# Kernel optimization log

Hardware: AMD Instinct MI355X
Metric: run time of the kernel (lower is better)

The kernel has to match this reference:

```python
import jax, jax.numpy as jnp
import numpy as np

PH, PW = 2, 2
SCALE = (0.5, 0.5)
HARDNESS = 2.0
BN_EPS = 1e-5

def conv2d(x, w, b, pad):
    y = jax.lax.conv_general_dilated(x, w, (1, 1), [(pad, pad), (pad, pad)],
                                     dimension_numbers=('NCHW', 'OIHW', 'NCHW'))
    return y + b[None, :, None, None]

def nearest_resize(x, oh, ow):
    # torch F.interpolate default 'nearest': src_idx = floor(dst_idx * in/out)
    _, _, ih, iw = x.shape
    hi = jnp.floor(jnp.arange(oh) * (ih / oh)).astype(jnp.int32)
    wi = jnp.floor(jnp.arange(ow) * (iw / ow)).astype(jnp.int32)
    return x[:, :, hi][:, :, :, wi]

def bilinear_resize(x, oh, ow):
    # matches torch bilinear align_corners=False (half-pixel, no antialias)
    b, c = x.shape[0], x.shape[1]
    return jax.image.resize(x, (b, c, oh, ow), method='linear', antialias=False)

def grid_sample_bilinear(feat, grid):
    # feat [B,C,H,W], grid [B,gh,gw,2] with (x,y) in [-1,1]; align_corners=False, zeros padding
    B, C, H, W = feat.shape
    gx, gy = grid[..., 0], grid[..., 1]
    ix = (gx + 1.0) * (W * 0.5) - 0.5
    iy = (gy + 1.0) * (H * 0.5) - 0.5
    x0f = jnp.floor(ix); y0f = jnp.floor(iy)
    wx = ix - x0f; wy = iy - y0f
    x0 = x0f.astype(jnp.int32); y0 = y0f.astype(jnp.int32)
    x1 = x0 + 1; y1 = y0 + 1

    def gather(f, yy, xx):
        valid = ((yy >= 0) & (yy < H) & (xx >= 0) & (xx < W)).astype(f.dtype)
        yc = jnp.clip(yy, 0, H - 1); xc = jnp.clip(xx, 0, W - 1)
        return f[:, yc, xc] * valid[None]  # [C,gh,gw]

    def per_sample(f, y0, x0, y1, x1, wx, wy):
        v00 = gather(f, y0, x0); v01 = gather(f, y0, x1)
        v10 = gather(f, y1, x0); v11 = gather(f, y1, x1)
        wx_ = wx[None]; wy_ = wy[None]
        return (v00 * (1 - wx_) * (1 - wy_) + v01 * wx_ * (1 - wy_)
                + v10 * (1 - wx_) * wy_ + v11 * wx_ * wy_)

    return jax.vmap(per_sample)(feat, y0, x0, y1, x1, wx, wy)

def lens_forward(feat, w1, b1, gamma, beta, rmean, rvar, w2, b2):
    B, C, H, W = feat.shape
    dh, dw = H // PH, W // PW
    dsz_h, dsz_w = int(H * SCALE[0]), int(W * SCALE[1])
    # ekern: conv3x3 + BN(eval) + ReLU6
    x = conv2d(feat, w1, b1, 1)
    inv = jax.lax.rsqrt(rvar + BN_EPS)
    x = (x - rmean[None, :, None, None]) * inv[None, :, None, None]
    x = x * gamma[None, :, None, None] + beta[None, :, None, None]
    x = jnp.clip(x, 0.0, 6.0)
    # dkern (eval branch): channel-norm normalize with gating, conv5x5 (no pad) + sigmoid
    nrm = jnp.linalg.norm(x, axis=1, keepdims=True)
    xn = x / (nrm + 9e-8) * (nrm > 0.09).astype(x.dtype)
    dmap_raw = jax.nn.sigmoid(conv2d(xn, w2, b2, 0))  # [B,2,H-4,W-4]
    ndmap = nearest_resize(dmap_raw, dh + 2, dw + 2)
    # dmap += 0.0009; interior += hardness
    mask = jnp.zeros((dh + 2, dw + 2), x.dtype).at[1:-1, 1:-1].set(1.0)
    dmap = ndmap + 0.0009 + HARDNESS * mask[None, None]
    # bilinear round trip through dsz
    dsm = bilinear_resize(dmap, dsz_h, dsz_w)
    dmap = bilinear_resize(dsm, dh + 2, dw + 2)
    # neko_dense_norm: normalize, cumsum -> CDF sampling grid in [-1,1]
    h_ = dmap[:, 0:1]; w_ = dmap[:, 1:2]
    h_ = h_ / jnp.sum(h_, axis=2, keepdims=True)
    w_ = w_ / jnp.sum(w_, axis=3, keepdims=True)
    hc = jnp.cumsum(h_, axis=2); wc = jnp.cumsum(w_, axis=3)
    grid = jnp.concatenate([wc[:, :, 1:-1, 1:-1], hc[:, :, 1:-1, 1:-1]], axis=1) * 2 - 1
    grid = jnp.transpose(grid, (0, 2, 3, 1))  # [B,dh,dw,2] (x,y)
    dst = grid_sample_bilinear(feat, grid)  # [B,C,dh,dw]
    # adaptive_avg_pool2d([dh,dw]) on a [dh,dw] map is identity -> skip
    return dst, dmap

def setup_inputs() -> dict:
    key = jax.random.key(0)
    ks = jax.random.split(key, 9)
    B, ICH, H, W, CH = 16, 64, 256, 256, 64
    feat = jax.random.normal(ks[0], (B, ICH, H, W), jnp.float32)
    w1 = jax.random.normal(ks[1], (CH, ICH, 3, 3), jnp.float32) * 0.05
    b1 = jax.random.normal(ks[2], (CH,), jnp.float32) * 0.05
    gamma = 1.0 + jax.random.normal(ks[3], (CH,), jnp.float32) * 0.05
    beta = jax.random.normal(ks[4], (CH,), jnp.float32) * 0.05
    rmean = jax.random.normal(ks[5], (CH,), jnp.float32) * 0.05
    rvar = jax.random.uniform(ks[6], (CH,), jnp.float32) + 0.5
    w2 = jax.random.normal(ks[7], (2, CH, 5, 5), jnp.float32) * 0.05
    b2 = jax.random.normal(ks[8], (2,), jnp.float32) * 0.05
    return {'feat': feat, 'w1': w1, 'b1': b1, 'gamma': gamma, 'beta': beta,
            'rmean': rmean, 'rvar': rvar, 'w2': w2, 'b2': b2}

def reference(feat, w1, b1, gamma, beta, rmean, rvar, w2, b2):
    dst, dmap = lens_forward(feat, w1, b1, gamma, beta, rmean, rvar, w2, b2)
    return dst, jax.lax.stop_gradient(dmap)
```

## Files before the change

kernel.cpp:

```cpp
#include <hip/hip_runtime.h>
#include <hip/hip_bf16.h>

typedef __hip_bfloat16 bf16;
typedef __attribute__((ext_vector_type(8))) short bf16x8;
typedef __attribute__((ext_vector_type(4))) float f32x4;

static __device__ __forceinline__ ushort f2bf(float f) {
    uint u = __float_as_uint(f);
    u += 0x7fff + ((u >> 16) & 1);
    return (ushort)(u >> 16);
}

static __device__ __forceinline__ void gl_lds16(const void* g, void* l) {
    __builtin_amdgcn_global_load_lds(
        (const __attribute__((address_space(1))) uint*)g,
        (__attribute__((address_space(3))) uint*)l, 16, 0, 0);
}

static __device__ __forceinline__ int xcd_remap(int lid, int nwg) {
    int q = nwg >> 3, r = nwg & 7;
    int xcd = lid & 7, idx = lid >> 3;
    return (xcd < r ? xcd * (q + 1) : r * (q + 1) + (xcd - r) * q) + idx;
}

#define FT_ROW 264
#define FT_IMG ((size_t)258 * 264 * 64)
#define XN_IMG ((size_t)256 * 256 * 64)

__global__ __launch_bounds__(256) void k_wt(const float* __restrict__ w1,
                                            ushort* __restrict__ w_bf) {
    int i = blockIdx.x * 256 + threadIdx.x;
    if (i >= 36864) return;
    int oc = i / 576, rem = i - oc * 576;
    int ic = rem / 9, tap = rem - ic * 9;
    w_bf[tap * 4096 + oc * 64 + (ic ^ ((oc & 7) << 3))] = f2bf(w1[i]);
}

__global__ __launch_bounds__(256) void k_wt2(const float* __restrict__ w2,
                                             ushort* __restrict__ w2_bf) {
    int i = blockIdx.x * 256 + threadIdx.x;
    if (i >= 3200) return;
    int oc = i / 1600, rem = i - oc * 1600;
    int ic = rem / 25, tap = rem - ic * 25;
    w2_bf[(tap * 2 + oc) * 64 + ic] = f2bf(w2[i]);
}

__global__ __launch_bounds__(256) void k_zero(ushort* __restrict__ featT, int nb) {
    int t = blockIdx.x * 256 + threadIdx.x;
    const int per = 1040 * 8;
    if (t >= nb * per) return;
    int b = t / per, u = t - b * per;
    int px = u >> 3, oct = u & 7;
    int yp, xp;
    if (px < 264)       { yp = 0;   xp = px; }
    else if (px < 528)  { yp = 257; xp = px - 264; }
    else { int k = px - 528; yp = 1 + (k >> 1); xp = (k & 1) ? 257 : 0; }
    ushort* p = featT + (size_t)b * FT_IMG + ((size_t)yp * FT_ROW + xp) * 64 + oct * 8;
    *(uint4*)p = make_uint4(0u, 0u, 0u, 0u);
}

__global__ __launch_bounds__(256) void k_tr(const float* __restrict__ feat_c,
                                            ushort* __restrict__ featT) {
    __shared__ ushort s_t[64][72];
    const int b = blockIdx.z, y = blockIdx.y, x0 = blockIdx.x * 64;
    const int t = threadIdx.x;
    const int xl = t & 63, icg = t >> 6;

    const float* fb = feat_c + (size_t)b * 64 * 65536 + (size_t)y * 256 + x0 + xl;
#pragma unroll
    for (int k = 0; k < 16; ++k) {
        int ic = icg * 16 + k;
        s_t[ic][xl] = f2bf(fb[(size_t)ic * 65536]);
    }
    __syncthreads();

    ushort* ob = featT + (size_t)b * FT_IMG + ((size_t)(y + 1) * FT_ROW + (x0 + 1)) * 64;
#pragma unroll
    for (int u2 = 0; u2 < 2; ++u2) {
        int u = u2 * 256 + t;
        int x = u >> 3, oct = u & 7;
        int xp7 = (x + 1) & 7;
        uint p0 = (uint)s_t[oct * 8 + 0][x] | ((uint)s_t[oct * 8 + 1][x] << 16);
        uint p1 = (uint)s_t[oct * 8 + 2][x] | ((uint)s_t[oct * 8 + 3][x] << 16);
        uint p2 = (uint)s_t[oct * 8 + 4][x] | ((uint)s_t[oct * 8 + 5][x] << 16);
        uint p3 = (uint)s_t[oct * 8 + 6][x] | ((uint)s_t[oct * 8 + 7][x] << 16);
        *(uint4*)(ob + (size_t)x * 64 + (oct ^ xp7) * 8) = make_uint4(p0, p1, p2, p3);
    }
}

__global__ __launch_bounds__(256, 2) void k_conv1(
    const ushort* __restrict__ featT, const ushort* __restrict__ w_bf,
    const float* __restrict__ b1, const float* __restrict__ gamma,
    const float* __restrict__ beta, const float* __restrict__ rmean,
    const float* __restrict__ rvar, ushort* __restrict__ xn) {
    __shared__ __align__(16) ushort s_in[6 * 72 * 64];
    __shared__ __align__(16) ushort s_w[12288];
    __shared__ float2 s_bn[64];

    const int lid = blockIdx.x + (blockIdx.y << 2) + (blockIdx.z << 8);
    const int nid = xcd_remap(lid, (int)gridDim.z << 8);
    const int b   = nid >> 8;
    const int x0p = (nid & 3) * 64;
    const int y0  = ((nid >> 2) & 63) * 4;

    const int tid = threadIdx.x;
    const int lane = tid & 63;
    const int w    = tid >> 6;
    const int l15  = lane & 15;
    const int l4   = lane >> 4;

    if (tid < 64) {
        float inv = 1.0f / sqrtf(rvar[tid] + 1e-5f);
        float sA = inv * gamma[tid];
        float sB = (b1[tid] - rmean[tid]) * sA + beta[tid];
        s_bn[tid] = make_float2(sA, sB);
    }

    const ushort* fT = featT + (size_t)b * FT_IMG;
    {
        int aStart = w * 13 + (w < 2 ? w : 2);
        int aCnt   = (w < 2) ? 14 : 13;
        for (int q = 0; q < aCnt; ++q) {
            int o = (aStart + q) * 1024;
            int r = o / 9216;
            int rem = o - r * 9216;
            const ushort* g = fT + ((size_t)(y0 + r) * FT_ROW + x0p) * 64 +
                              (rem >> 1) + lane * 8;
            gl_lds16(g, (char*)s_in + o);
        }
    }

    f32x4 acc[4][4];
#pragma unroll
    for (int m = 0; m < 4; m++)
#pragma unroll
        for (int n = 0; n < 4; n++) acc[m][n] = (f32x4){0.f, 0.f, 0.f, 0.f};

    for (int dy = 0; dy < 3; dy++) {
        __syncthreads();
        {
            for (int q = 0; q < 6; ++q) {
                int o = (w * 6 + q) * 1024;
                const ushort* g = w_bf + dy * 12288 + (o >> 1) + lane * 8;
                gl_lds16(g, (char*)s_w + o);
            }
        }
        __syncthreads();
#pragma unroll
        for (int dx = 0; dx < 3; dx++) {
#pragma unroll
            for (int ks = 0; ks < 2; ks++) {
                bf16x8 a[4], bb[4];
#pragma unroll
                for (int m = 0; m < 4; m++) {
                    int c = m * 16 + l15 + dx;
                    int slot = (ks * 4 + l4) ^ (c & 7);
                    a[m] = *(const bf16x8*)&s_in[((w + dy) * 72 + c) * 64 + slot * 8];
                }
#pragma unroll
                for (int n = 0; n < 4; n++) {
                    int oc = n * 16 + l15;
                    int slot = (ks * 4 + l4) ^ (oc & 7);
                    bb[n] = *(const bf16x8*)&s_w[(dx * 64 + oc) * 64 + slot * 8];
                }
#pragma unroll
                for (int m = 0; m < 4; m++)
#pragma unroll
                    for (int n = 0; n < 4; n++)
                        acc[m][n] = __builtin_amdgcn_mfma_f32_16x16x32_bf16(
                            bb[n], a[m], acc[m][n], 0, 0, 0);
            }
        }
    }

    float sA[4][4], sB[4][4];
#pragma unroll
    for (int n = 0; n < 4; n++)
#pragma unroll
        for (int j = 0; j < 4; j++) {
            float2 t = s_bn[n * 16 + l4 * 4 + j];
            sA[n][j] = t.x; sB[n][j] = t.y;
        }
    const int y = y0 + w;
    ushort* xb = xn + (size_t)b * XN_IMG;

#pragma unroll
    for (int m = 0; m < 4; m++) {
        float vv[4][4];
        float ss = 0.f;
#pragma unroll
        for (int n = 0; n < 4; n++)
#pragma unroll
            for (int j = 0; j < 4; j++) {
                float v = fmaf(acc[m][n][j], sA[n][j], sB[n][j]);
                v = fminf(fmaxf(v, 0.f), 6.f);
                vv[n][j] = v;
                ss = fmaf(v, v, ss);
            }
        ss += __shfl_xor(ss, 16);
        ss += __shfl_xor(ss, 32);
        float nrm = sqrtf(ss);
        float sc = (nrm > 0.09f) ? (1.0f / (nrm + 9e-8f)) : 0.f;

        int x = x0p + m * 16 + l15;
        ushort* pb = xb + ((size_t)y * 256 + x) * 64;
        int so = (l4 & 1) * 4;
#pragma unroll
        for (int n = 0; n < 4; n++) {
            int oct = n * 2 + (l4 >> 1);
            int slot = oct ^ (x & 7);
            uint2 pk;
            pk.x = (uint)f2bf(vv[n][0] * sc) | ((uint)f2bf(vv[n][1] * sc) << 16);
            pk.y = (uint)f2bf(vv[n][2] * sc) | ((uint)f2bf(vv[n][3] * sc) << 16);
            *(uint2*)(pb + slot * 8 + so) = pk;
        }
    }
}

__global__ __launch_bounds__(256, 2) void k_conv2(
    const ushort* __restrict__ xn, const ushort* __restrict__ w2_bf,
    const float* __restrict__ b2, float* __restrict__ dmap_raw2) {
    __shared__ __align__(16) ushort s_in[11 * 80 * 32];

    const int lid = blockIdx.x + (blockIdx.y << 2) + blockIdx.z * 132;
    const int nid = xcd_remap(lid, (int)gridDim.z * 132);
    const int b   = nid / 132;
    const int rem = nid - b * 132;
    const int x0  = (rem & 3) * 64;
    const int oy0 = (rem >> 2) * 4;

    const int tid = threadIdx.x;
    const int lane = tid & 63;
    const int w    = tid >> 6;
    const int l15  = lane & 15;
    const int l4   = lane >> 4;

    const float SC = (float)(252.0 / 130.0);
    const int syb = (int)floorf((float)oy0 * SC);
    const int oy  = oy0 + w;
    const int syrel = (int)floorf((float)oy * SC) - syb;

    const ushort* xb = xn + (size_t)b * XN_IMG;

    f32x4 acc[4];
#pragma unroll
    for (int n = 0; n < 4; n++) acc[n] = (f32x4){0.f, 0.f, 0.f, 0.f};

    for (int c = 0; c < 2; ++c) {
        if (c) __syncthreads();
        {
            int st  = (w < 3) ? w * 14 : 42;
            int cnt = (w < 3) ? 14 : 13;
            for (int q = 0; q < cnt; ++q) {
                int i = st + q;
                int r = i / 5;
                int px0 = (i - r * 5) * 16;
                int gr = min(syb + r, 255);
                int px = px0 + (lane >> 2);
                int gx = x0 + px;
                const ushort* g = xb + (size_t)(gr * 256 + gx) * 64 +
                                  ((((gx >> 2) & 1) ^ c) * 32) + (lane & 3) * 8;
                gl_lds16(g, (char*)s_in + i * 1024);
            }
        }
        __syncthreads();

#pragma unroll
        for (int dy = 0; dy < 5; dy++) {
#pragma unroll
            for (int dx = 0; dx < 5; dx++) {
                bf16x8 aw;
                if (l15 < 2)
                    aw = *(const bf16x8*)(w2_bf + ((dy * 5 + dx) * 2 + l15) * 64 +
                                          c * 32 + l4 * 8);
                else
                    aw = (bf16x8){0, 0, 0, 0, 0, 0, 0, 0};
                bf16x8 bx[4];
#pragma unroll
                for (int n = 0; n < 4; n++) {
                    int px = n * 16 + l15 + dx;
                    int slot4 = l4 ^ (px & 3);
                    bx[n] = *(const bf16x8*)&s_in[((syrel + dy) * 80 + px) * 32 + slot4 * 8];
                }
#pragma unroll
                for (int n = 0; n < 4; n++)
                    acc[n] = __builtin_amdgcn_mfma_f32_16x16x32_bf16(
                        aw, bx[n], acc[n], 0, 0, 0);
            }
        }
    }

    if (l4 == 0 && oy < 130) {
        float bias0 = b2[0], bias1 = b2[1];
#pragma unroll
        for (int n = 0; n < 4; n++) {
            int ox = x0 + n * 16 + l15;
            if (ox < 252) {
                float v0 = acc[n][0] + bias0;
                float v1 = acc[n][1] + bias1;
                size_t o = (size_t)b * 65520 + (size_t)oy * 252 + ox;
                dmap_raw2[o] = 1.f / (1.f + expf(-v0));
                dmap_raw2[o + 32760] = 1.f / (1.f + expf(-v1));
            }
        }
    }
}

__global__ __launch_bounds__(256) void k_dmap(const float* __restrict__ dmap_raw2,
                                              float* __restrict__ out_dmap,
                                              float* __restrict__ grid) {
    __shared__ float sA[16900];
    __shared__ float sB[16384];
    const int ch = blockIdx.x, b = blockIdx.y;
    const int tid = threadIdx.x;
    const float SC = (float)(252.0 / 130.0);

    const float* src = dmap_raw2 + (size_t)b * 65520 + (size_t)ch * 32760;
    for (int i = tid; i < 16900; i += 256) {
        int oy = i / 130, ox = i - oy * 130;
        int sx = (int)floorf((float)ox * SC);
        float m = (oy >= 1 && oy <= 128 && ox >= 1 && ox <= 128) ? 2.0f : 0.0f;
        sA[i] = src[oy * 252 + sx] + 0.0009f + m;
    }
    __syncthreads();

    {
        const float sc = (float)(130.0 / 128.0);
        for (int i = tid; i < 16384; i += 256) {
            int oy = i >> 7, ox = i & 127;
            float sy = ((float)oy + 0.5f) * sc - 0.5f;
            float sx = ((float)ox + 0.5f) * sc - 0.5f;
            float y0f = floorf(sy), x0f = floorf(sx);
            float wy = sy - y0f, wx = sx - x0f;
            int y0 = max(min((int)y0f, 129), 0), y1 = max(min((int)y0f + 1, 129), 0);
            int x0 = max(min((int)x0f, 129), 0), x1 = max(min((int)x0f + 1, 129), 0);
            float top = sA[y0 * 130 + x0] * (1.f - wx) + sA[y0 * 130 + x1] * wx;
            float bot = sA[y1 * 130 + x0] * (1.f - wx) + sA[y1 * 130 + x1] * wx;
            sB[i] = top * (1.f - wy) + bot * wy;
        }
    }
    __syncthreads();

    {
        const float sc = (float)(128.0 / 130.0);
        float* od = out_dmap + ((size_t)b * 2 + ch) * 16900;
        for (int i = tid; i < 16900; i += 256) {
            int oy = i / 130, ox = i - oy * 130;
            float sy = ((float)oy + 0.5f) * sc - 0.5f;
            float sx = ((float)ox + 0.5f) * sc - 0.5f;
            float y0f = floorf(sy), x0f = floorf(sx);
            float wy = sy - y0f, wx = sx - x0f;
            int y0 = max(min((int)y0f, 127), 0), y1 = max(min((int)y0f + 1, 127), 0);
            int x0 = max(min((int)x0f, 127), 0), x1 = max(min((int)x0f + 1, 127), 0);
            float top = sB[y0 * 128 + x0] * (1.f - wx) + sB[y0 * 128 + x1] * wx;
            float bot = sB[y1 * 128 + x0] * (1.f - wx) + sB[y1 * 128 + x1] * wx;
            float v = top * (1.f - wy) + bot * wy;
            od[i] = v;
            sA[i] = v;
        }
    }
    __syncthreads();

    if (tid < 130) {
        float* g = grid + (size_t)b * 32768;
        if (ch == 0) {
            float s = 0.f;
            for (int r = 0; r < 130; r++) s += sA[r * 130 + tid];
            float inv = 1.f / s;
            float cs = 0.f;
            for (int r = 0; r < 130; r++) {
                cs += sA[r * 130 + tid] * inv;
                if (r >= 1 && r <= 128 && tid >= 1 && tid <= 128)
                    g[((r - 1) * 128 + (tid - 1)) * 2 + 1] = cs * 2.f - 1.f;
            }
        } else {
            const float* row = sA + tid * 130;
            float s = 0.f;
            for (int x = 0; x < 130; x++) s += row[x];
            float inv = 1.f / s;
            float cs = 0.f;
            for (int x = 0; x < 130; x++) {
                cs += row[x] * inv;
                if (x >= 1 && x <= 128 && tid >= 1 && tid <= 128)
                    g[((tid - 1) * 128 + (x - 1)) * 2 + 0] = cs * 2.f - 1.f;
            }
        }
    }
}

__global__ __launch_bounds__(256) void k_sample(const float* __restrict__ feat_c,
                                                const float* __restrict__ grid,
                                                float* __restrict__ dst_c) {
    const int b = blockIdx.z;
    const int x = blockIdx.x * 16 + (threadIdx.x & 15);
    const int y = blockIdx.y * 16 + (threadIdx.x >> 4);

    const float* g = grid + (((size_t)b * 128 + y) * 128 + x) * 2;
    float gx = g[0], gy = g[1];
    float ix = (gx + 1.f) * 128.f - 0.5f;
    float iy = (gy + 1.f) * 128.f - 0.5f;
    float x0f = floorf(ix), y0f = floorf(iy);
    float wx = ix - x0f, wy = iy - y0f;
    int ix0 = (int)x0f, iy0 = (int)y0f;
    int ix1 = ix0 + 1, iy1 = iy0 + 1;
    float vx0 = ((unsigned)ix0 < 256u) ? 1.f : 0.f;
    float vx1 = ((unsigned)ix1 < 256u) ? 1.f : 0.f;
    float vy0 = ((unsigned)iy0 < 256u) ? 1.f : 0.f;
    float vy1 = ((unsigned)iy1 < 256u) ? 1.f : 0.f;
    int cx0 = max(min(ix0, 255), 0), cx1 = max(min(ix1, 255), 0);
    int cy0 = max(min(iy0, 255), 0), cy1 = max(min(iy1, 255), 0);
    float w00 = (1.f - wx) * (1.f - wy) * vx0 * vy0;
    float w01 = wx * (1.f - wy) * vx1 * vy0;
    float w10 = (1.f - wx) * wy * vx0 * vy1;
    float w11 = wx * wy * vx1 * vy1;

    const float* fb = feat_c + (size_t)b * 64 * 65536;
    int o00 = cy0 * 256 + cx0, o01 = cy0 * 256 + cx1;
    int o10 = cy1 * 256 + cx0, o11 = cy1 * 256 + cx1;
    float* d = dst_c + (size_t)b * 64 * 16384 + (size_t)y * 128 + x;
#pragma unroll 4
    for (int c = 0; c < 64; c++) {
        const float* fc = fb + (size_t)c * 65536;
        d[(size_t)c * 16384] = fc[o00] * w00 + fc[o01] * w01 +
                               fc[o10] * w10 + fc[o11] * w11;
    }
}

static inline size_t align256(size_t x) { return (x + 255) & ~(size_t)255; }

extern "C" void kernel_launch(void* const* d_in, const int* in_sizes, int n_in,
                              void* d_out, int out_size, void* d_ws, size_t ws_size,
                              hipStream_t stream) {
    const float* feat  = (const float*)d_in[0];
    const float* w1    = (const float*)d_in[1];
    const float* b1    = (const float*)d_in[2];
    const float* gamma = (const float*)d_in[3];
    const float* beta  = (const float*)d_in[4];
    const float* rmean = (const float*)d_in[5];
    const float* rvar  = (const float*)d_in[6];
    const float* w2    = (const float*)d_in[7];
    const float* b2    = (const float*)d_in[8];

    float* out = (float*)d_out;
    float* out_dst  = out;
    float* out_dmap = out + 16777216;

    int nb = 1;
    const int cands[5] = {16, 8, 4, 2, 1};
    for (int k = 0; k < 5; ++k) {
        int n = cands[k];
        size_t need = align256((size_t)n * FT_IMG * 2)
                    + align256((size_t)n * XN_IMG * 2)
                    + align256(73728)
                    + align256(12800)
                    + align256((size_t)n * 65520 * 4)
                    + align256((size_t)n * 131072);
        if (need <= ws_size) { nb = n; break; }
    }

    char* p = (char*)d_ws;
    ushort* featT    = (ushort*)p; p += align256((size_t)nb * FT_IMG * 2);
    ushort* xn       = (ushort*)p; p += align256((size_t)nb * XN_IMG * 2);
    ushort* w_bf     = (ushort*)p; p += align256(73728);
    ushort* w2_bf    = (ushort*)p; p += align256(12800);
    float* dmap_raw2 = (float*)p;  p += align256((size_t)nb * 65520 * 4);
    float* grid      = (float*)p;

    k_wt<<<144, 256, 0, stream>>>(w1, w_bf);
    k_wt2<<<13, 256, 0, stream>>>(w2, w2_bf);

    const int nchunks = 16 / nb;
    for (int c = 0; c < nchunks; ++c) {
        const float* feat_c = feat + (size_t)c * nb * 64 * 65536;
        float* dst_c  = out_dst  + (size_t)c * nb * 64 * 16384;
        float* dmap_c = out_dmap + (size_t)c * nb * 2 * 16900;

        k_zero<<<(nb * 8320 + 255) / 256, 256, 0, stream>>>(featT, nb);
        k_tr<<<dim3(4, 256, nb), 256, 0, stream>>>(feat_c, featT);
        k_conv1<<<dim3(4, 64, nb), 256, 0, stream>>>(featT, w_bf, b1, gamma,
                                                     beta, rmean, rvar, xn);
        k_conv2<<<dim3(4, 33, nb), 256, 0, stream>>>(xn, w2_bf, b2, dmap_raw2);
        k_dmap<<<dim3(2, nb), 256, 0, stream>>>(dmap_raw2, dmap_c, grid);
        k_sample<<<dim3(8, 8, nb), 256, 0, stream>>>(feat_c, grid, dst_c);
    }
}
```

Measured before the change: 407.4 us.

## Read conv1 weights from global, shrink LDS tile, merge prep kernels

The conv1 kernel no longer stages weight taps through shared memory. B fragments are loaded straight from global/L2 memory, which removes the two barriers per dy step and most of the LDS footprint. The input halo tile shrinks from 72 to 66 columns (64 columns via LDS DMA plus a small direct copy), and launch bounds rise to 3 blocks per CU. The weight transforms and the border zeroing are merged into one prep kernel that runs once instead of per chunk. The risk is higher global load latency inside the MFMA loop, plus register pressure from the tighter launch bound.

```diff
diff --git a/kernel.cpp b/kernel.cpp
--- a/kernel.cpp
+++ b/kernel.cpp
@@ -27,36 +27,34 @@
 #define FT_IMG ((size_t)258 * 264 * 64)
 #define XN_IMG ((size_t)256 * 256 * 64)
 
-__global__ __launch_bounds__(256) void k_wt(const float* __restrict__ w1,
-                                            ushort* __restrict__ w_bf) {
+__global__ __launch_bounds__(256) void k_prep(const float* __restrict__ w1,
+                                              const float* __restrict__ w2,
+                                              ushort* __restrict__ w_bf,
+                                              ushort* __restrict__ w2_bf,
+                                              ushort* __restrict__ featT, int nb) {
     int i = blockIdx.x * 256 + threadIdx.x;
-    if (i >= 36864) return;
-    int oc = i / 576, rem = i - oc * 576;
-    int ic = rem / 9, tap = rem - ic * 9;
-    w_bf[tap * 4096 + oc * 64 + (ic ^ ((oc & 7) << 3))] = f2bf(w1[i]);
-}
-
-__global__ __launch_bounds__(256) void k_wt2(const float* __restrict__ w2,
-                                             ushort* __restrict__ w2_bf) {
-    int i = blockIdx.x * 256 + threadIdx.x;
-    if (i >= 3200) return;
-    int oc = i / 1600, rem = i - oc * 1600;
-    int ic = rem / 25, tap = rem - ic * 25;
-    w2_bf[(tap * 2 + oc) * 64 + ic] = f2bf(w2[i]);
-}
-
-__global__ __launch_bounds__(256) void k_zero(ushort* __restrict__ featT, int nb) {
-    int t = blockIdx.x * 256 + threadIdx.x;
-    const int per = 1040 * 8;
-    if (t >= nb * per) return;
-    int b = t / per, u = t - b * per;
-    int px = u >> 3, oct = u & 7;
-    int yp, xp;
-    if (px < 264)       { yp = 0;   xp = px; }
-    else if (px < 528)  { yp = 257; xp = px - 264; }
-    else { int k = px - 528; yp = 1 + (k >> 1); xp = (k & 1) ? 257 : 0; }
-    ushort* p = featT + (size_t)b * FT_IMG + ((size_t)yp * FT_ROW + xp) * 64 + oct * 8;
-    *(uint4*)p = make_uint4(0u, 0u, 0u, 0u);
+    if (i < 36864) {
+        int oc = i / 576, rem = i - oc * 576;
+        int ic = rem / 9, tap = rem - ic * 9;
+        w_bf[tap * 4096 + oc * 64 + ic] = f2bf(w1[i]);
+    } else if (i < 40064) {
+        int j = i - 36864;
+        int oc = j / 1600, rem = j - oc * 1600;
+        int ic = rem / 25, tap = rem - ic * 25;
+        w2_bf[(tap * 2 + oc) * 64 + ic] = f2bf(w2[j]);
+    } else {
+        int t = i - 40064;
+        const int per = 1040 * 8;
+        if (t >= nb * per) return;
+        int b = t / per, u = t - b * per;
+        int px = u >> 3, oct = u & 7;
+        int yp, xp;
+        if (px < 264)       { yp = 0;   xp = px; }
+        else if (px < 528)  { yp = 257; xp = px - 264; }
+        else { int k = px - 528; yp = 1 + (k >> 1); xp = (k & 1) ? 257 : 0; }
+        ushort* p = featT + (size_t)b * FT_IMG + ((size_t)yp * FT_ROW + xp) * 64 + oct * 8;
+        *(uint4*)p = make_uint4(0u, 0u, 0u, 0u);
+    }
 }
 
 __global__ __launch_bounds__(256) void k_tr(const float* __restrict__ feat_c,
@@ -88,13 +86,12 @@
     }
 }
 
-__global__ __launch_bounds__(256, 2) void k_conv1(
+__global__ __launch_bounds__(256, 3) void k_conv1(
     const ushort* __restrict__ featT, const ushort* __restrict__ w_bf,
     const float* __restrict__ b1, const float* __restrict__ gamma,
     const float* __restrict__ beta, const float* __restrict__ rmean,
     const float* __restrict__ rvar, ushort* __restrict__ xn) {
-    __shared__ __align__(16) ushort s_in[6 * 72 * 64];
-    __shared__ __align__(16) ushort s_w[12288];
+    __shared__ __align__(16) ushort s_in[6 * 66 * 64];
     __shared__ float2 s_bn[64];
 
     const int lid = blockIdx.x + (blockIdx.y << 2) + (blockIdx.z << 8);
@@ -117,18 +114,20 @@
     }
 
     const ushort* fT = featT + (size_t)b * FT_IMG;
-    {
-        int aStart = w * 13 + (w < 2 ? w : 2);
-        int aCnt   = (w < 2) ? 14 : 13;
-        for (int q = 0; q < aCnt; ++q) {
-            int o = (aStart + q) * 1024;
-            int r = o / 9216;
-            int rem = o - r * 9216;
-            const ushort* g = fT + ((size_t)(y0 + r) * FT_ROW + x0p) * 64 +
-                              (rem >> 1) + lane * 8;
-            gl_lds16(g, (char*)s_in + o);
-        }
-    }
+    for (int q = 0; q < 12; ++q) {
+        int f = w * 12 + q;
+        int r = f >> 3, seg = f & 7;
+        const ushort* g = fT + ((size_t)(y0 + r) * FT_ROW + x0p) * 64 +
+                          seg * 512 + lane * 8;
+        gl_lds16(g, (char*)s_in + r * 8448 + seg * 1024);
+    }
+    if (tid < 96) {
+        int r = tid >> 4, t16 = tid & 15;
+        const uint4 v = *(const uint4*)(fT + ((size_t)(y0 + r) * FT_ROW + x0p + 64) * 64 +
+                                        t16 * 8);
+        *(uint4*)((char*)s_in + r * 8448 + 8192 + t16 * 16) = v;
+    }
+    __syncthreads();
 
     f32x4 acc[4][4];
 #pragma unroll
@@ -136,16 +135,8 @@
 #pragma unroll
         for (int n = 0; n < 4; n++) acc[m][n] = (f32x4){0.f, 0.f, 0.f, 0.f};
 
+#pragma unroll
     for (int dy = 0; dy < 3; dy++) {
-        __syncthreads();
-        {
-            for (int q = 0; q < 6; ++q) {
-                int o = (w * 6 + q) * 1024;
-                const ushort* g = w_bf + dy * 12288 + (o >> 1) + lane * 8;
-                gl_lds16(g, (char*)s_w + o);
-            }
-        }
-        __syncthreads();
 #pragma unroll
         for (int dx = 0; dx < 3; dx++) {
 #pragma unroll
@@ -155,13 +146,13 @@
                 for (int m = 0; m < 4; m++) {
                     int c = m * 16 + l15 + dx;
                     int slot = (ks * 4 + l4) ^ (c & 7);
-                    a[m] = *(const bf16x8*)&s_in[((w + dy) * 72 + c) * 64 + slot * 8];
+                    a[m] = *(const bf16x8*)&s_in[((w + dy) * 66 + c) * 64 + slot * 8];
                 }
 #pragma unroll
                 for (int n = 0; n < 4; n++) {
                     int oc = n * 16 + l15;
-                    int slot = (ks * 4 + l4) ^ (oc & 7);
-                    bb[n] = *(const bf16x8*)&s_w[(dx * 64 + oc) * 64 + slot * 8];
+                    bb[n] = *(const bf16x8*)(w_bf + (dy * 3 + dx) * 4096 +
+                                             oc * 64 + ks * 32 + l4 * 8);
                 }
 #pragma unroll
                 for (int m = 0; m < 4; m++)
@@ -466,8 +457,8 @@
     float* dmap_raw2 = (float*)p;  p += align256((size_t)nb * 65520 * 4);
     float* grid      = (float*)p;
 
-    k_wt<<<144, 256, 0, stream>>>(w1, w_bf);
-    k_wt2<<<13, 256, 0, stream>>>(w2, w2_bf);
+    k_prep<<<(40064 + nb * 8320 + 255) / 256, 256, 0, stream>>>(
+        w1, w2, w_bf, w2_bf, featT, nb);
 
     const int nchunks = 16 / nb;
     for (int c = 0; c < nchunks; ++c) {
@@ -475,7 +466,6 @@
         float* dst_c  = out_dst  + (size_t)c * nb * 64 * 16384;
         float* dmap_c = out_dmap + (size_t)c * nb * 2 * 16900;
 
-        k_zero<<<(nb * 8320 + 255) / 256, 256, 0, stream>>>(featT, nb);
         k_tr<<<dim3(4, 256, nb), 256, 0, stream>>>(feat_c, featT);
         k_conv1<<<dim3(4, 64, nb), 256, 0, stream>>>(featT, w_bf, b1, gamma,
                                                      beta, rmean, rvar, xn);
```

Measured after the change: 494.1 us. 21.3% more time.
